# Kernel tuning notes

Measured on AMD Instinct MI355X. Metric: run time of the kernel, lower is better.

## Reference

```python
import jax, jax.numpy as jnp
import numpy as np

LN_EPS = 1e-5


def setup_inputs() -> dict:
    key = jax.random.key(0)
    k1, k2, k3, k4 = jax.random.split(key, 4)
    bs, len_a, len_b, h = 32, 300, 1024, 512
    return {
        "feat_a": jax.random.normal(k1, (bs, len_a, h), dtype=jnp.float32),
        "feat_b": jax.random.normal(k2, (bs, len_b, h), dtype=jnp.float32),
        "W": jax.random.normal(k3, (h, h, h), dtype=jnp.float32),  # [out, in1, in2] like nn.Bilinear
        "bias": jax.random.normal(k4, (h,), dtype=jnp.float32),
        "gamma": jnp.ones((h,), dtype=jnp.float32),
        "beta": jnp.zeros((h,), dtype=jnp.float32),
    }


def reference(feat_a, feat_b, W, bias, gamma, beta):
    # mean_j bilinear(a_i, b_j) == bilinear(a_i, mean_j b_j): bilinear is linear in b,
    # bias is constant over j -> exact same math as expand+Bilinear+mean in the source.
    b_mean = jnp.mean(feat_b, axis=1)                      # [bs, h]
    t = jnp.einsum('kde,be->bkd', W, b_mean)               # [bs, h_out, h_in1]
    fused = jnp.einsum('bad,bkd->bak', feat_a, t) + bias   # [bs, len_a, h]
    # dropout is identity in eval mode
    x = fused + feat_a
    mu = jnp.mean(x, axis=-1, keepdims=True)
    var = jnp.mean(jnp.square(x - mu), axis=-1, keepdims=True)
    xn = (x - mu) * jax.lax.rsqrt(var + LN_EPS)
    return xn * gamma + beta
```

## Files before the change

kernel.cpp:

```cpp
#include <hip/hip_runtime.h>

#define LN_EPS 1e-5f

typedef short s8v __attribute__((ext_vector_type(8)));
typedef float f4v __attribute__((ext_vector_type(4)));

constexpr int BS = 32, LA = 300, LB = 1024, H = 512;
constexpr long RTOT = (long)H * H;


union U8 { s8v v; unsigned u[4]; };
union FU { float f; unsigned u; };

__device__ inline unsigned pack_hi16(unsigned a, unsigned b) {
  return (a >> 16) | (b & 0xffff0000u);
}

__device__ inline void split8(const f4v w0, const f4v w1, s8v& hi, s8v& lo) {
  FU f[8] = {{w0.x}, {w0.y}, {w0.z}, {w0.w}, {w1.x}, {w1.y}, {w1.z}, {w1.w}};
  U8 h, l;
#pragma unroll
  for (int p = 0; p < 4; ++p) {
    const unsigned ua = f[2 * p].u, ub = f[2 * p + 1].u;
    h.u[p] = pack_hi16(ua, ub);
    FU ra, rb;
    ra.f = f[2 * p].f - __uint_as_float(ua & 0xffff0000u);
    rb.f = f[2 * p + 1].f - __uint_as_float(ub & 0xffff0000u);
    l.u[p] = pack_hi16(ra.u, rb.u);
  }
  hi = h.v;
  lo = l.v;
}

__global__ __launch_bounds__(512) void k_bmean_part(const float* __restrict__ fb,
                                                    float* __restrict__ part) {
  const int b = blockIdx.x >> 3, c = blockIdx.x & 7;
  const int e = threadIdx.x;
  const float* src = fb + ((long)b * LB + (long)c * 128) * H + e;
  float s = 0.f;
#pragma unroll 8
  for (int j = 0; j < 128; ++j) s += __builtin_nontemporal_load(&src[(long)j * H]);
  part[((b << 3) + c) * H + e] = s;
}

__global__ __launch_bounds__(512) void k_bmean_final(const float* __restrict__ part,
                                                     unsigned short* __restrict__ bmh,
                                                     unsigned short* __restrict__ bml) {
  const int b = blockIdx.x, e = threadIdx.x;
  float s = 0.f;
#pragma unroll
  for (int c = 0; c < 8; ++c) s += part[((b << 3) + c) * H + e];
  const float v = s * (1.f / LB);
  FU u; u.f = v;
  bmh[b * H + e] = (unsigned short)(u.u >> 16);
  FU r; r.f = v - __uint_as_float(u.u & 0xffff0000u);
  bml[b * H + e] = (unsigned short)(r.u >> 16);
}

__global__ __launch_bounds__(256) void k_wt(const float* __restrict__ W,
                                            const unsigned short* __restrict__ bmh,
                                            const unsigned short* __restrict__ bml,
                                            unsigned short* __restrict__ thi,
                                            unsigned short* __restrict__ tlo) {
  const int tid = threadIdx.x, wv = tid >> 6, ln = tid & 63;
  const int l16 = ln & 15, kg = ln >> 4;
  const long r0 = (long)blockIdx.x * 256 + wv * 64;

  f4v acc[2][4];
#pragma unroll
  for (int m = 0; m < 2; ++m)
#pragma unroll
    for (int n = 0; n < 4; ++n) acc[m][n] = (f4v){0.f, 0.f, 0.f, 0.f};

  const float* wp = W + (r0 + l16) * (long)H + kg * 8;
  const int aoff = l16 * H + kg * 8;

#define LOADW(W0, W1, E)                                          \
  _Pragma("unroll")                                               \
  for (int nt = 0; nt < 4; ++nt) {                                \
    const f4v* p = (const f4v*)(wp + (long)nt * 16 * H + (E));    \
    W0[nt] = __builtin_nontemporal_load(p);                       \
    W1[nt] = __builtin_nontemporal_load(p + 1);                   \
  }

#define COMPUTEW(W0, W1, E)                                                                \
  {                                                                                        \
    const s8v ah0 = *(const s8v*)(bmh + aoff + (E));                                       \
    const s8v al0 = *(const s8v*)(bml + aoff + (E));                                       \
    const s8v ah1 = *(const s8v*)(bmh + 16 * H + aoff + (E));                              \
    const s8v al1 = *(const s8v*)(bml + 16 * H + aoff + (E));                              \
    _Pragma("unroll")                                                                      \
    for (int nt = 0; nt < 4; ++nt) {                                                       \
      s8v wh, wl;                                                                          \
      split8(W0[nt], W1[nt], wh, wl);                                                      \
      acc[0][nt] = __builtin_amdgcn_mfma_f32_16x16x32_bf16(ah0, wh, acc[0][nt], 0, 0, 0);  \
      acc[0][nt] = __builtin_amdgcn_mfma_f32_16x16x32_bf16(al0, wh, acc[0][nt], 0, 0, 0);  \
      acc[0][nt] = __builtin_amdgcn_mfma_f32_16x16x32_bf16(ah0, wl, acc[0][nt], 0, 0, 0);  \
      acc[1][nt] = __builtin_amdgcn_mfma_f32_16x16x32_bf16(ah1, wh, acc[1][nt], 0, 0, 0);  \
      acc[1][nt] = __builtin_amdgcn_mfma_f32_16x16x32_bf16(al1, wh, acc[1][nt], 0, 0, 0);  \
      acc[1][nt] = __builtin_amdgcn_mfma_f32_16x16x32_bf16(ah1, wl, acc[1][nt], 0, 0, 0);  \
    }                                                                                      \
  }

  f4v wa0[4], wa1[4], wb0[4], wb1[4];
  LOADW(wa0, wa1, 0);
  for (int e0 = 0; e0 < H; e0 += 64) {
    LOADW(wb0, wb1, e0 + 32);
    COMPUTEW(wa0, wa1, e0);
    if (e0 + 64 < H) LOADW(wa0, wa1, e0 + 64);
    COMPUTEW(wb0, wb1, e0 + 32);
  }
#undef LOADW
#undef COMPUTEW

#pragma unroll
  for (int m = 0; m < 2; ++m)
#pragma unroll
    for (int nt = 0; nt < 4; ++nt)
#pragma unroll
      for (int j = 0; j < 4; ++j) {
        const float v = acc[m][nt][j];
        const long idx = (long)(m * 16 + kg * 4 + j) * RTOT + r0 + nt * 16 + l16;
        FU u; u.f = v;
        thi[idx] = (unsigned short)(u.u >> 16);
        FU r; r.f = v - __uint_as_float(u.u & 0xffff0000u);
        tlo[idx] = (unsigned short)(r.u >> 16);
      }
}

__global__ __launch_bounds__(256) void k_fused(const float* __restrict__ fa,
                                               const unsigned short* __restrict__ thi,
                                               const unsigned short* __restrict__ tlo,
                                               float* __restrict__ out) {
  const int tid = threadIdx.x, wv = tid >> 6, ln = tid & 63;
  const int l16 = ln & 15, kg = ln >> 4;
  const int b = blockIdx.z, a0 = blockIdx.y * 64, k0 = blockIdx.x * 128 + wv * 32;

  f4v acc[4][2];
#pragma unroll
  for (int m = 0; m < 4; ++m)
#pragma unroll
    for (int n = 0; n < 2; ++n) acc[m][n] = (f4v){0.f, 0.f, 0.f, 0.f};

  const float* fab = fa + (long)b * LA * H;
  const unsigned short* th = thi + (long)b * RTOT;
  const unsigned short* tl = tlo + (long)b * RTOT;

  for (int d0 = 0; d0 < H; d0 += 32) {
    s8v afh[4], afl[4];
#pragma unroll
    for (int mt = 0; mt < 4; ++mt) {
      int a = a0 + mt * 16 + l16;
      if (a > LA - 1) a = LA - 1;
      const float* p = fab + (long)a * H + d0 + kg * 8;
      const f4v w0 = *(const f4v*)p;
      const f4v w1 = *(const f4v*)(p + 4);
      split8(w0, w1, afh[mt], afl[mt]);
    }
#pragma unroll
    for (int nt = 0; nt < 2; ++nt) {
      const long boff = (long)(k0 + nt * 16 + l16) * H + d0 + kg * 8;
      const s8v bh = *(const s8v*)(th + boff);
      const s8v bl = *(const s8v*)(tl + boff);
#pragma unroll
      for (int mt = 0; mt < 4; ++mt) {
        acc[mt][nt] = __builtin_amdgcn_mfma_f32_16x16x32_bf16(afh[mt], bh, acc[mt][nt], 0, 0, 0);
        acc[mt][nt] = __builtin_amdgcn_mfma_f32_16x16x32_bf16(afl[mt], bh, acc[mt][nt], 0, 0, 0);
        acc[mt][nt] = __builtin_amdgcn_mfma_f32_16x16x32_bf16(afh[mt], bl, acc[mt][nt], 0, 0, 0);
      }
    }
  }
#pragma unroll
  for (int mt = 0; mt < 4; ++mt)
#pragma unroll
    for (int nt = 0; nt < 2; ++nt)
#pragma unroll
      for (int j = 0; j < 4; ++j) {
        const int a = a0 + mt * 16 + kg * 4 + j;
        if (a < LA)
          out[((long)b * LA + a) * H + k0 + nt * 16 + l16] = acc[mt][nt][j];
      }
}

__global__ __launch_bounds__(64) void k_ln(const float* __restrict__ fa,
                                           const float* __restrict__ bias,
                                           const float* __restrict__ gamma,
                                           const float* __restrict__ beta,
                                           float* __restrict__ out) {
  const long row = blockIdx.x;
  const int tid = threadIdx.x;
  float* fr = out + row * H;
  const float* ar = fa + row * H;
  float x[8];
  float s = 0.f, ss = 0.f;
#pragma unroll
  for (int q = 0; q < 2; ++q) {
    const int k = (q << 8) + (tid << 2);
    const float4 f = *(const float4*)&fr[k];
    const float4 a = *(const float4*)&ar[k];
    const float4 bi = *(const float4*)&bias[k];
    x[q * 4 + 0] = f.x + a.x + bi.x;
    x[q * 4 + 1] = f.y + a.y + bi.y;
    x[q * 4 + 2] = f.z + a.z + bi.z;
    x[q * 4 + 3] = f.w + a.w + bi.w;
#pragma unroll
    for (int u = 0; u < 4; ++u) { s += x[q * 4 + u]; ss += x[q * 4 + u] * x[q * 4 + u]; }
  }
#pragma unroll
  for (int o = 32; o; o >>= 1) { s += __shfl_xor(s, o); ss += __shfl_xor(ss, o); }
  const float mu = s * (1.f / H);
  const float var = ss * (1.f / H) - mu * mu;
  const float rs = rsqrtf(var + LN_EPS);
#pragma unroll
  for (int q = 0; q < 2; ++q) {
    const int k = (q << 8) + (tid << 2);
    const float4 g = *(const float4*)&gamma[k];
    const float4 be = *(const float4*)&beta[k];
    float4 o;
    o.x = (x[q * 4 + 0] - mu) * rs * g.x + be.x;
    o.y = (x[q * 4 + 1] - mu) * rs * g.y + be.y;
    o.z = (x[q * 4 + 2] - mu) * rs * g.z + be.z;
    o.w = (x[q * 4 + 3] - mu) * rs * g.w + be.w;
    *(float4*)&fr[k] = o;
  }
}

extern "C" void kernel_launch(void* const* d_in, const int* in_sizes, int n_in,
                              void* d_out, int out_size, void* d_ws, size_t ws_size,
                              hipStream_t stream) {
  const float* fa = (const float*)d_in[0];
  const float* fb = (const float*)d_in[1];
  const float* W = (const float*)d_in[2];
  const float* bias = (const float*)d_in[3];
  const float* gamma = (const float*)d_in[4];
  const float* beta = (const float*)d_in[5];
  float* out = (float*)d_out;
  char* ws = (char*)d_ws;

  float* part = (float*)ws;
  unsigned short* bmh = (unsigned short*)(ws + 524288);
  unsigned short* bml = (unsigned short*)(ws + 557056);
  unsigned short* thi = (unsigned short*)(ws + 589824);
  unsigned short* tlo = (unsigned short*)(ws + 589824 + 16777216);

  hipLaunchKernelGGL(k_bmean_part, dim3(256), dim3(512), 0, stream, fb, part);
  hipLaunchKernelGGL(k_bmean_final, dim3(32), dim3(512), 0, stream, part, bmh, bml);
  hipLaunchKernelGGL(k_wt, dim3((int)(RTOT / 256)), dim3(256), 0, stream, W, bmh, bml, thi, tlo);
  hipLaunchKernelGGL(k_fused, dim3(4, 5, 32), dim3(256), 0, stream, fa, thi, tlo, out);
  hipLaunchKernelGGL(k_ln, dim3(BS * LA), dim3(64), 0, stream, fa, bias, gamma, beta, out);
}
```

Measured before the change: 838.6 us.

## Fuse LayerNorm epilogue into batched GEMM with full-row block tiles

The GEMM kernel is retiled so each block covers 32 rows and all 512 output columns, four waves each taking 128 columns. That lets bias, residual add and LayerNorm run in the epilogue, with row sums reduced through shuffles and shared memory. The separate LN kernel goes away, along with the round trip of the fused intermediate through global memory. The grid shrinks from 640 to 320 blocks and each wave holds more accumulators, which may hurt occupancy and latency hiding. The variance is still computed as E[x^2]-mu^2.

```diff
diff --git a/kernel.cpp b/kernel.cpp
--- a/kernel.cpp
+++ b/kernel.cpp
@@ -128,28 +128,33 @@
       }
 }
 
-__global__ __launch_bounds__(256) void k_fused(const float* __restrict__ fa,
-                                               const unsigned short* __restrict__ thi,
-                                               const unsigned short* __restrict__ tlo,
-                                               float* __restrict__ out) {
+__global__ __launch_bounds__(256) void k_fused_ln(const float* __restrict__ fa,
+                                                  const unsigned short* __restrict__ thi,
+                                                  const unsigned short* __restrict__ tlo,
+                                                  const float* __restrict__ bias,
+                                                  const float* __restrict__ gamma,
+                                                  const float* __restrict__ beta,
+                                                  float* __restrict__ out) {
   const int tid = threadIdx.x, wv = tid >> 6, ln = tid & 63;
   const int l16 = ln & 15, kg = ln >> 4;
-  const int b = blockIdx.z, a0 = blockIdx.y * 64, k0 = blockIdx.x * 128 + wv * 32;
-
-  f4v acc[4][2];
-#pragma unroll
-  for (int m = 0; m < 4; ++m)
-#pragma unroll
-    for (int n = 0; n < 2; ++n) acc[m][n] = (f4v){0.f, 0.f, 0.f, 0.f};
+  const int b = blockIdx.y, a0 = blockIdx.x * 32, k0 = wv * 128;
+
+  __shared__ float sums[4][32], ssq[4][32];
+
+  f4v acc[2][8];
+#pragma unroll
+  for (int m = 0; m < 2; ++m)
+#pragma unroll
+    for (int n = 0; n < 8; ++n) acc[m][n] = (f4v){0.f, 0.f, 0.f, 0.f};
 
   const float* fab = fa + (long)b * LA * H;
   const unsigned short* th = thi + (long)b * RTOT;
   const unsigned short* tl = tlo + (long)b * RTOT;
 
   for (int d0 = 0; d0 < H; d0 += 32) {
-    s8v afh[4], afl[4];
-#pragma unroll
-    for (int mt = 0; mt < 4; ++mt) {
+    s8v afh[2], afl[2];
+#pragma unroll
+    for (int mt = 0; mt < 2; ++mt) {
       int a = a0 + mt * 16 + l16;
       if (a > LA - 1) a = LA - 1;
       const float* p = fab + (long)a * H + d0 + kg * 8;
@@ -158,71 +163,80 @@
       split8(w0, w1, afh[mt], afl[mt]);
     }
 #pragma unroll
-    for (int nt = 0; nt < 2; ++nt) {
+    for (int nt = 0; nt < 8; ++nt) {
       const long boff = (long)(k0 + nt * 16 + l16) * H + d0 + kg * 8;
       const s8v bh = *(const s8v*)(th + boff);
       const s8v bl = *(const s8v*)(tl + boff);
 #pragma unroll
-      for (int mt = 0; mt < 4; ++mt) {
+      for (int mt = 0; mt < 2; ++mt) {
         acc[mt][nt] = __builtin_amdgcn_mfma_f32_16x16x32_bf16(afh[mt], bh, acc[mt][nt], 0, 0, 0);
         acc[mt][nt] = __builtin_amdgcn_mfma_f32_16x16x32_bf16(afl[mt], bh, acc[mt][nt], 0, 0, 0);
         acc[mt][nt] = __builtin_amdgcn_mfma_f32_16x16x32_bf16(afh[mt], bl, acc[mt][nt], 0, 0, 0);
       }
     }
   }
-#pragma unroll
-  for (int mt = 0; mt < 4; ++mt)
-#pragma unroll
-    for (int nt = 0; nt < 2; ++nt)
-#pragma unroll
-      for (int j = 0; j < 4; ++j) {
-        const int a = a0 + mt * 16 + kg * 4 + j;
-        if (a < LA)
-          out[((long)b * LA + a) * H + k0 + nt * 16 + l16] = acc[mt][nt][j];
-      }
-}
-
-__global__ __launch_bounds__(64) void k_ln(const float* __restrict__ fa,
-                                           const float* __restrict__ bias,
-                                           const float* __restrict__ gamma,
-                                           const float* __restrict__ beta,
-                                           float* __restrict__ out) {
-  const long row = blockIdx.x;
-  const int tid = threadIdx.x;
-  float* fr = out + row * H;
-  const float* ar = fa + row * H;
-  float x[8];
-  float s = 0.f, ss = 0.f;
-#pragma unroll
-  for (int q = 0; q < 2; ++q) {
-    const int k = (q << 8) + (tid << 2);
-    const float4 f = *(const float4*)&fr[k];
-    const float4 a = *(const float4*)&ar[k];
-    const float4 bi = *(const float4*)&bias[k];
-    x[q * 4 + 0] = f.x + a.x + bi.x;
-    x[q * 4 + 1] = f.y + a.y + bi.y;
-    x[q * 4 + 2] = f.z + a.z + bi.z;
-    x[q * 4 + 3] = f.w + a.w + bi.w;
-#pragma unroll
-    for (int u = 0; u < 4; ++u) { s += x[q * 4 + u]; ss += x[q * 4 + u] * x[q * 4 + u]; }
-  }
-#pragma unroll
-  for (int o = 32; o; o >>= 1) { s += __shfl_xor(s, o); ss += __shfl_xor(ss, o); }
-  const float mu = s * (1.f / H);
-  const float var = ss * (1.f / H) - mu * mu;
-  const float rs = rsqrtf(var + LN_EPS);
-#pragma unroll
-  for (int q = 0; q < 2; ++q) {
-    const int k = (q << 8) + (tid << 2);
-    const float4 g = *(const float4*)&gamma[k];
-    const float4 be = *(const float4*)&beta[k];
-    float4 o;
-    o.x = (x[q * 4 + 0] - mu) * rs * g.x + be.x;
-    o.y = (x[q * 4 + 1] - mu) * rs * g.y + be.y;
-    o.z = (x[q * 4 + 2] - mu) * rs * g.z + be.z;
-    o.w = (x[q * 4 + 3] - mu) * rs * g.w + be.w;
-    *(float4*)&fr[k] = o;
-  }
+
+  float bval[8], gval[8], beval[8];
+#pragma unroll
+  for (int nt = 0; nt < 8; ++nt) {
+    const int k = k0 + nt * 16 + l16;
+    bval[nt] = bias[k];
+    gval[nt] = gamma[k];
+    beval[nt] = beta[k];
+  }
+#pragma unroll
+  for (int mt = 0; mt < 2; ++mt)
+#pragma unroll
+    for (int j = 0; j < 4; ++j) {
+      int a = a0 + mt * 16 + kg * 4 + j;
+      if (a > LA - 1) a = LA - 1;
+      const float* far = fab + (long)a * H;
+#pragma unroll
+      for (int nt = 0; nt < 8; ++nt)
+        acc[mt][nt][j] += bval[nt] + far[k0 + nt * 16 + l16];
+    }
+
+#pragma unroll
+  for (int mt = 0; mt < 2; ++mt)
+#pragma unroll
+    for (int j = 0; j < 4; ++j) {
+      float s = 0.f, ss = 0.f;
+#pragma unroll
+      for (int nt = 0; nt < 8; ++nt) {
+        const float v = acc[mt][nt][j];
+        s += v;
+        ss += v * v;
+      }
+#pragma unroll
+      for (int o = 1; o < 16; o <<= 1) { s += __shfl_xor(s, o); ss += __shfl_xor(ss, o); }
+      if (l16 == 0) {
+        sums[wv][mt * 16 + kg * 4 + j] = s;
+        ssq[wv][mt * 16 + kg * 4 + j] = ss;
+      }
+    }
+  __syncthreads();
+
+#pragma unroll
+  for (int mt = 0; mt < 2; ++mt)
+#pragma unroll
+    for (int j = 0; j < 4; ++j) {
+      const int rt = mt * 16 + kg * 4 + j;
+      float S = 0.f, SS = 0.f;
+#pragma unroll
+      for (int w = 0; w < 4; ++w) { S += sums[w][rt]; SS += ssq[w][rt]; }
+      const float mu = S * (1.f / H);
+      const float var = SS * (1.f / H) - mu * mu;
+      const float rs = rsqrtf(var + LN_EPS);
+      const int a = a0 + rt;
+      if (a < LA) {
+        float* orow = out + ((long)b * LA + a) * H;
+#pragma unroll
+        for (int nt = 0; nt < 8; ++nt) {
+          const int k = k0 + nt * 16 + l16;
+          orow[k] = (acc[mt][nt][j] - mu) * rs * gval[nt] + beval[nt];
+        }
+      }
+    }
 }
 
 extern "C" void kernel_launch(void* const* d_in, const int* in_sizes, int n_in,
@@ -246,6 +260,5 @@
   hipLaunchKernelGGL(k_bmean_part, dim3(256), dim3(512), 0, stream, fb, part);
   hipLaunchKernelGGL(k_bmean_final, dim3(32), dim3(512), 0, stream, part, bmh, bml);
   hipLaunchKernelGGL(k_wt, dim3((int)(RTOT / 256)), dim3(256), 0, stream, W, bmh, bml, thi, tlo);
-  hipLaunchKernelGGL(k_fused, dim3(4, 5, 32), dim3(256), 0, stream, fa, thi, tlo, out);
-  hipLaunchKernelGGL(k_ln, dim3(BS * LA), dim3(64), 0, stream, fa, bias, gamma, beta, out);
-}
+  hipLaunchKernelGGL(k_fused_ln, dim3(10, 32), dim3(256), 0, stream, fa, thi, tlo, bias, gamma, beta, out);
+}
```

Result: slower. 860.7 us (+2.6%).
